# Performance work log

Measured on AMD Instinct MI355X. Metric: run time of the kernel, lower is better.

The kernel has to match this reference:

```python
import jax, jax.numpy as jnp
import numpy as np

B, N, D = 16, 512, 256   # batch, tokens(=input_size), emb_dim
H, DH = 8, 16            # heads, dim_head
INNER = H * DH           # 128
SCALE = DH ** -0.5
EPS = 1e-5


def _p(key, shape):
    return jax.random.normal(key, shape, dtype=jnp.float32) * 0.02


def setup_inputs() -> dict:
    key = jax.random.key(0)
    ks = jax.random.split(key, 12)
    inp = {
        "x": jax.random.normal(ks[0], (B, N, D), dtype=jnp.float32),
        # stage-1 attention (tokens=N, feat=D)
        "wqkv1": _p(ks[1], (D, 3 * INNER)),
        "wo1": _p(ks[2], (INNER, D)),
        "bo1": jnp.zeros((D,), jnp.float32),
        "ff1_w1": _p(ks[3], (D, 8 * D)),
        "ff1_b1": jnp.zeros((8 * D,), jnp.float32),
        "ff1_w2": _p(ks[4], (4 * D, D)),
        "ff1_b2": jnp.zeros((D,), jnp.float32),
        # stage-2 attention (tokens=D after transpose, feat=N=input_size)
        "wqkv2": _p(ks[5], (N, 3 * INNER)),
        "wo2": _p(ks[6], (INNER, N)),
        "bo2": jnp.zeros((N,), jnp.float32),
        "ff2_w1": _p(ks[7], (N, 8 * N)),
        "ff2_b1": jnp.zeros((8 * N,), jnp.float32),
        "ff2_w2": _p(ks[8], (4 * N, N)),
        "ff2_b2": jnp.zeros((N,), jnp.float32),
        # layernorms
        "ln1_g": jnp.ones((D,), jnp.float32), "ln1_b": jnp.zeros((D,), jnp.float32),
        "ln2_g": jnp.ones((D,), jnp.float32), "ln2_b": jnp.zeros((D,), jnp.float32),
        "ln3_g": jnp.ones((N,), jnp.float32), "ln3_b": jnp.zeros((N,), jnp.float32),
        "ln4_g": jnp.ones((N,), jnp.float32), "ln4_b": jnp.zeros((N,), jnp.float32),
    }
    return inp


def _layernorm(x, g, b):
    mu = jnp.mean(x, axis=-1, keepdims=True)
    var = jnp.mean(jnp.square(x - mu), axis=-1, keepdims=True)
    return (x - mu) * jax.lax.rsqrt(var + EPS) * g + b


def _attention(x, wqkv, wo, bo, share):
    b, n, _ = x.shape
    qkv = x @ wqkv                                 # [b, n, 3*INNER]
    q, k, v = jnp.split(qkv, 3, axis=-1)
    split_heads = lambda t: t.reshape(b, n, H, DH).transpose(0, 2, 1, 3)
    q, k, v = split_heads(q), split_heads(k), split_heads(v)
    energy = jnp.einsum('bhid,bhjd->bhij', q, k) * SCALE
    if share is not None:
        energy = energy + share
    attn = jax.nn.softmax(energy, axis=-1)
    out = jnp.einsum('bhij,bhjd->bhid', attn, v)   # [b, h, n, dh]
    out = out.transpose(0, 2, 1, 3).reshape(b, n, INNER)
    return out @ wo + bo, energy


def _geglu_ff(x, w1, b1, w2, b2):
    h = x @ w1 + b1
    a, g = jnp.split(h, 2, axis=-1)
    return (a * jax.nn.gelu(g, approximate=False)) @ w2 + b2


def reference(x, wqkv1, wo1, bo1, ff1_w1, ff1_b1, ff1_w2, ff1_b2,
              wqkv2, wo2, bo2, ff2_w1, ff2_b1, ff2_w2, ff2_b2,
              ln1_g, ln1_b, ln2_g, ln2_b, ln3_g, ln3_b, ln4_g, ln4_b):
    # stage 1: token attention + FFN
    attn_out, share = _attention(x, wqkv1, wo1, bo1, None)
    x = _layernorm(attn_out + x, ln1_g, ln1_b)
    x = _layernorm(_geglu_ff(x, ff1_w1, ff1_b1, ff1_w2, ff1_b2) + x, ln2_g, ln2_b)
    # stage 2: feature (column) attention + FFN on transposed x
    x = x.transpose(0, 2, 1)                       # [b, D, N]
    attn_out, share2 = _attention(x, wqkv2, wo2, bo2, None)
    x = _layernorm(attn_out + x, ln3_g, ln3_b)
    x = _layernorm(_geglu_ff(x, ff2_w1, ff2_b1, ff2_w2, ff2_b2) + x, ln4_g, ln4_b)
    x = x.transpose(0, 2, 1)                       # [b, N, D]
    return (x, share, share2)
```

## Files before the change

### kernel.cpp

```cpp
#include <hip/hip_runtime.h>
#include <cstddef>


typedef __attribute__((ext_vector_type(8))) short short8;
typedef __attribute__((ext_vector_type(4))) short bf16x4;
typedef __attribute__((ext_vector_type(4))) float f32x4;
typedef unsigned short u16t;

__device__ __forceinline__ u16t f2b(float f) {
  union { float f; unsigned u; } x; x.f = f;
  unsigned r = (x.u + 0x7fffu + ((x.u >> 16) & 1u)) >> 16;
  return (u16t)r;
}
__device__ __forceinline__ float b2f(u16t v) {
  union { unsigned u; float f; } x; x.u = ((unsigned)v) << 16;
  return x.f;
}

__device__ __forceinline__ void gload16(const void* g, void* l) {
  __builtin_amdgcn_global_load_lds(
      (const __attribute__((address_space(1))) void*)g,
      (__attribute__((address_space(3))) void*)l, 16, 0, 0);
}

__device__ __forceinline__ int origcol(int n, int halfN) {
  const int nb = n >> 7, s = (n >> 4) & 7, r = n & 15;
  return ((s & 1) ? halfN : 0) + (nb << 6) + ((s >> 1) << 4) + r;
}

template<int BN, int EPI>
__global__ __launch_bounds__(256) void mgemm(
    const u16t* __restrict__ A, const u16t* __restrict__ BT,
    const float* __restrict__ bias, const float* __restrict__ res,
    void* __restrict__ C, int M, int N, int K) {
  constexpr int WGC = (BN == 128) ? 2 : 1;
  constexpr int WM = (WGC == 2) ? 64 : 32;
  constexpr int MR = WM / 16;
  constexpr int NR = 4;
  constexpr int BISS = BN / 64;
  __shared__ u16t Al[128 * 32];
  __shared__ u16t Bl[BN * 32];
  const int t = threadIdx.x, lane = t & 63, wid = t >> 6;
  const int wr = (WGC == 2) ? (wid >> 1) : wid;
  const int wc = (WGC == 2) ? (wid & 1) : 0;
  const int lr = lane & 15, lq = lane >> 4;
  const int bm = blockIdx.y << 7, bn = blockIdx.x * BN;

  const int ao0 = wid * 2048 + lane * 16;
  const int ar0 = ao0 >> 6,          ac0 = (ao0 & 63) >> 1;
  const int ar1 = (ao0 + 1024) >> 6, ac1 = ((ao0 + 1024) & 63) >> 1;
  const int bo0 = wid * (1024 * BISS) + lane * 16;
  const int br0 = bo0 >> 6,          bc0 = (bo0 & 63) >> 1;
  const int br1 = (bo0 + 1024) >> 6, bc1 = ((bo0 + 1024) & 63) >> 1;

  const u16t* Ab = A + (size_t)bm * K;
  const u16t* Bb = BT + (size_t)bn * K;

  f32x4 acc[MR][NR];
#pragma unroll
  for (int m = 0; m < MR; ++m)
#pragma unroll
    for (int n = 0; n < NR; ++n) acc[m][n] = (f32x4){0.f, 0.f, 0.f, 0.f};

  for (int k0 = 0; k0 < K; k0 += 32) {
    gload16(Ab + (size_t)ar0 * K + k0 + ac0, (char*)Al + wid * 2048);
    gload16(Ab + (size_t)ar1 * K + k0 + ac1, (char*)Al + wid * 2048 + 1024);
    gload16(Bb + (size_t)br0 * K + k0 + bc0, (char*)Bl + wid * 1024 * BISS);
    if (BISS == 2)
      gload16(Bb + (size_t)br1 * K + k0 + bc1, (char*)Bl + wid * 2048 + 1024);
    __syncthreads();
    short8 af[MR], bf[NR];
#pragma unroll
    for (int m = 0; m < MR; ++m)
      af[m] = *(const short8*)&Al[(wr * WM + m * 16 + lr) * 32 + lq * 8];
#pragma unroll
    for (int n = 0; n < NR; ++n)
      bf[n] = *(const short8*)&Bl[(wc * 64 + n * 16 + lr) * 32 + lq * 8];
#pragma unroll
    for (int m = 0; m < MR; ++m)
#pragma unroll
      for (int n = 0; n < NR; ++n)
        acc[m][n] = __builtin_amdgcn_mfma_f32_16x16x32_bf16(af[m], bf[n], acc[m][n], 0, 0, 0);
    __syncthreads();
  }

  if (EPI == 2) {
    const int Nh = N >> 1;
#pragma unroll
    for (int np = 0; np < NR / 2; ++np) {
      const int ca = bn + wc * 64 + np * 32 + lr;
      const float ba = bias[ca], bg = bias[ca + 16];
      const int uc = (bn >> 1) + wc * 32 + np * 16 + lr;
#pragma unroll
      for (int m = 0; m < MR; ++m) {
#pragma unroll
        for (int i = 0; i < 4; ++i) {
          const int row = bm + wr * WM + m * 16 + lq * 4 + i;
          const float a = acc[m][2 * np][i] + ba;
          const float g = acc[m][2 * np + 1][i] + bg;
          const float ge = 0.5f * g * (1.f + erff(g * 0.70710678118654752f));
          ((u16t*)C)[(size_t)row * Nh + uc] = f2b(a * ge);
        }
      }
    }
  } else {
#pragma unroll
    for (int n = 0; n < NR; ++n) {
      const int col = bn + wc * 64 + n * 16 + lr;
      const float bv = bias ? bias[col] : 0.f;
#pragma unroll
      for (int m = 0; m < MR; ++m) {
#pragma unroll
        for (int i = 0; i < 4; ++i) {
          const int row = bm + wr * WM + m * 16 + lq * 4 + i;
          float v = acc[m][n][i] + bv;
          if (EPI == 1) {
            v += res[(size_t)row * N + col];
            ((float*)C)[(size_t)row * N + col] = v;
          } else {
            ((u16t*)C)[(size_t)row * N + col] = f2b(v);
          }
        }
      }
    }
  }
}

template<int NTOK>
__global__ __launch_bounds__(256) void attn_mfma(
    const u16t* __restrict__ qkv, float* __restrict__ share,
    u16t* __restrict__ outb) {
  __shared__ u16t VT[16][NTOK + 40];
  __shared__ u16t PB[4][16][40];
  const int t = threadIdx.x, lane = t & 63, wv = t >> 6;
  const int lr = lane & 15, lq = lane >> 4;
  const int bpb = NTOK / 64;
  const int bh = blockIdx.x / bpb, rg = blockIdx.x % bpb;
  const int b = bh >> 3, h = bh & 7;
  const u16t* qkvb = qkv + (size_t)b * NTOK * 384;

  for (int tok = t; tok < NTOK; tok += 256) {
    const u16t* vp = qkvb + (size_t)tok * 384 + 256 + h * 16;
    short8 v0 = *(const short8*)vp;
    short8 v1 = *(const short8*)(vp + 8);
#pragma unroll
    for (int d = 0; d < 8; ++d) {
      VT[d][tok]     = (u16t)v0[d];
      VT[d + 8][tok] = (u16t)v1[d];
    }
  }
  __syncthreads();

  const int i0 = rg * 64 + wv * 16;
  short8 qf = {0, 0, 0, 0, 0, 0, 0, 0};
  if (lq < 2)
    qf = *(const short8*)(qkvb + (size_t)(i0 + lr) * 384 + h * 16 + lq * 8);

  f32x4 oacc = {0.f, 0.f, 0.f, 0.f};
  f32x4 sacc = {0.f, 0.f, 0.f, 0.f};
  const f32x4 zero = {0.f, 0.f, 0.f, 0.f};
  float* shb = share + (size_t)bh * NTOK * NTOK;

  for (int t0 = 0; t0 < NTOK; t0 += 32) {
#pragma unroll
    for (int s2 = 0; s2 < 2; ++s2) {
      short8 kf = {0, 0, 0, 0, 0, 0, 0, 0};
      if (lq < 2)
        kf = *(const short8*)(qkvb + (size_t)(t0 + s2 * 16 + lr) * 384 + 128 + h * 16 + lq * 8);
      f32x4 e = __builtin_amdgcn_mfma_f32_16x16x32_bf16(qf, kf, zero, 0, 0, 0);
#pragma unroll
      for (int i = 0; i < 4; ++i) {
        const float ev = e[i] * 0.25f;
        shb[(size_t)(i0 + lq * 4 + i) * NTOK + t0 + s2 * 16 + lr] = ev;
        const float p = __expf(ev);
        sacc[i] += p;
        PB[wv][lq * 4 + i][s2 * 16 + lr] = f2b(p);
      }
    }
    asm volatile("s_waitcnt lgkmcnt(0)" ::: "memory");
    __builtin_amdgcn_sched_barrier(0);
    short8 pa = *(const short8*)&PB[wv][lr][lq * 8];
    short8 vf = *(const short8*)&VT[lr][t0 + lq * 8];
    oacc = __builtin_amdgcn_mfma_f32_16x16x32_bf16(pa, vf, oacc, 0, 0, 0);
    __builtin_amdgcn_sched_barrier(0);
  }
#pragma unroll
  for (int i = 0; i < 4; ++i) {
    float s = sacc[i];
    s += __shfl_xor(s, 1); s += __shfl_xor(s, 2);
    s += __shfl_xor(s, 4); s += __shfl_xor(s, 8);
    sacc[i] = s;
  }
#pragma unroll
  for (int i = 0; i < 4; ++i) {
    const float o = oacc[i] / sacc[i];
    outb[((size_t)(b * NTOK) + i0 + lq * 4 + i) * 128 + h * 16 + lr] = f2b(o);
  }
}

template<int NT, bool B16>
__global__ __launch_bounds__(NT) void ln_vec(
    const float* __restrict__ xin, const float* __restrict__ g,
    const float* __restrict__ be, float* __restrict__ y32,
    u16t* __restrict__ y16, int D) {
  const int row = blockIdx.x, t = threadIdx.x;
  const int lane = t & 63;
  const float4 x = ((const float4*)xin)[(size_t)row * (D >> 2) + t];
  float s = x.x + x.y + x.z + x.w;
  float s2 = x.x * x.x + x.y * x.y + x.z * x.z + x.w * x.w;
#pragma unroll
  for (int off = 32; off; off >>= 1) {
    s  += __shfl_xor(s, off);
    s2 += __shfl_xor(s2, off);
  }
  if (NT == 128) {
    __shared__ float a1[2], a2[2];
    const int wv = t >> 6;
    if (lane == 0) { a1[wv] = s; a2[wv] = s2; }
    __syncthreads();
    s = a1[0] + a1[1]; s2 = a2[0] + a2[1];
  }
  const float mean = s / D;
  const float var  = s2 / D - mean * mean;
  const float rstd = rsqrtf(var + 1e-5f);
  const float4 gv = ((const float4*)g)[t];
  const float4 bv = ((const float4*)be)[t];
  float4 y;
  y.x = (x.x - mean) * rstd * gv.x + bv.x;
  y.y = (x.y - mean) * rstd * gv.y + bv.y;
  y.z = (x.z - mean) * rstd * gv.z + bv.z;
  y.w = (x.w - mean) * rstd * gv.w + bv.w;
  ((float4*)y32)[(size_t)row * (D >> 2) + t] = y;
  if (B16) {
    bf16x4 p;
    p[0] = (short)f2b(y.x); p[1] = (short)f2b(y.y);
    p[2] = (short)f2b(y.z); p[3] = (short)f2b(y.w);
    *(bf16x4*)&y16[(size_t)row * D + t * 4] = p;
  }
}

template<bool BF16OUT>
__global__ void transp(const float* __restrict__ in, float* __restrict__ out32,
                       u16t* __restrict__ out16, int R, int C) {
  __shared__ float tile[32][33];
  const int b = blockIdx.z;
  const int r0 = blockIdx.y << 5, c0 = blockIdx.x << 5;
  const float* inb = in + (size_t)b * R * C;
  const int tx = threadIdx.x, ty = threadIdx.y;
#pragma unroll
  for (int dy = 0; dy < 32; dy += 8)
    tile[ty + dy][tx] = inb[(size_t)(r0 + ty + dy) * C + c0 + tx];
  __syncthreads();
#pragma unroll
  for (int dy = 0; dy < 32; dy += 8) {
    const float v = tile[tx][ty + dy];
    const size_t idx = (size_t)b * R * C + (size_t)(c0 + ty + dy) * R + r0 + tx;
    out32[idx] = v;
    if (BF16OUT) out16[idx] = f2b(v);
  }
}

__global__ __launch_bounds__(256) void prep_all(
    const float* __restrict__ x0, u16t* __restrict__ x16,
    const float* __restrict__ wqkv1, u16t* __restrict__ tqkv1,
    const float* __restrict__ wo1,   u16t* __restrict__ two1,
    const float* __restrict__ ff1w1, u16t* __restrict__ tff1a,
    const float* __restrict__ ff1w2, u16t* __restrict__ tff1b,
    const float* __restrict__ wqkv2, u16t* __restrict__ tqkv2,
    const float* __restrict__ wo2,   u16t* __restrict__ two2,
    const float* __restrict__ ff2w1, u16t* __restrict__ tff2a,
    const float* __restrict__ ff2w2, u16t* __restrict__ tff2b,
    const float* __restrict__ ff1b1, float* __restrict__ bp1,
    const float* __restrict__ ff2b1, float* __restrict__ bp2) {
  __shared__ float tile[32][33];
  const int b = blockIdx.x, t = threadIdx.x;
  const int tx = t & 31, ty = t >> 5;
  const float* src; u16t* dst;
  int K, N, bxd, blk, halfN = 0; bool perm = false;
  if (b < 1024) {
    const float* p = x0 + (size_t)(b * 256 + t) * 8;
    short8 v;
#pragma unroll
    for (int j = 0; j < 8; ++j) v[j] = (short)f2b(p[j]);
    *(short8*)(x16 + (size_t)(b * 256 + t) * 8) = v;
    return;
  } else if (b < 1120) { src = wqkv1; dst = tqkv1; K = 256;  N = 384;  bxd = 12;  blk = b - 1024; }
  else if (b < 1152)   { src = wo1;   dst = two1;  K = 128;  N = 256;  bxd = 8;   blk = b - 1120; }
  else if (b < 1664)   { src = ff1w1; dst = tff1a; K = 256;  N = 2048; bxd = 64;  blk = b - 1152; perm = true; halfN = 1024; }
  else if (b < 1920)   { src = ff1w2; dst = tff1b; K = 1024; N = 256;  bxd = 8;   blk = b - 1664; }
  else if (b < 2112)   { src = wqkv2; dst = tqkv2; K = 512;  N = 384;  bxd = 12;  blk = b - 1920; }
  else if (b < 2176)   { src = wo2;   dst = two2;  K = 128;  N = 512;  bxd = 16;  blk = b - 2112; }
  else if (b < 4224)   { src = ff2w1; dst = tff2a; K = 512;  N = 4096; bxd = 128; blk = b - 2176; perm = true; halfN = 2048; }
  else if (b < 5248)   { src = ff2w2; dst = tff2b; K = 2048; N = 512;  bxd = 16;  blk = b - 4224; }
  else if (b < 5256) { const int n = (b - 5248) * 256 + t; bp1[n] = ff1b1[origcol(n, 1024)]; return; }
  else               { const int n = (b - 5256) * 256 + t; bp2[n] = ff2b1[origcol(n, 2048)]; return; }

  const int bx = blk % bxd, by = blk / bxd;
  const int n0 = bx * 32, k0 = by * 32;
  const int nn = n0 + tx;
  const int no = perm ? origcol(nn, halfN) : nn;
#pragma unroll
  for (int dy = 0; dy < 32; dy += 8)
    tile[ty + dy][tx] = src[(size_t)(k0 + ty + dy) * N + no];
  __syncthreads();
#pragma unroll
  for (int dy = 0; dy < 32; dy += 8)
    dst[(size_t)(n0 + ty + dy) * K + k0 + tx] = f2b(tile[tx][ty + dy]);
}

extern "C" void kernel_launch(void* const* d_in, const int* in_sizes, int n_in,
                              void* d_out, int out_size, void* d_ws, size_t ws_size,
                              hipStream_t stream) {
  (void)in_sizes; (void)n_in; (void)out_size; (void)ws_size;
  const float* x0    = (const float*)d_in[0];
  const float* wqkv1 = (const float*)d_in[1];
  const float* wo1   = (const float*)d_in[2];
  const float* bo1   = (const float*)d_in[3];
  const float* ff1w1 = (const float*)d_in[4];
  const float* ff1b1 = (const float*)d_in[5];
  const float* ff1w2 = (const float*)d_in[6];
  const float* ff1b2 = (const float*)d_in[7];
  const float* wqkv2 = (const float*)d_in[8];
  const float* wo2   = (const float*)d_in[9];
  const float* bo2   = (const float*)d_in[10];
  const float* ff2w1 = (const float*)d_in[11];
  const float* ff2b1 = (const float*)d_in[12];
  const float* ff2w2 = (const float*)d_in[13];
  const float* ff2b2 = (const float*)d_in[14];
  const float* ln1g  = (const float*)d_in[15];
  const float* ln1b  = (const float*)d_in[16];
  const float* ln2g  = (const float*)d_in[17];
  const float* ln2b  = (const float*)d_in[18];
  const float* ln3g  = (const float*)d_in[19];
  const float* ln3b  = (const float*)d_in[20];
  const float* ln4g  = (const float*)d_in[21];
  const float* ln4b  = (const float*)d_in[22];

  float* out_x  = (float*)d_out;
  float* share1 = out_x + (size_t)2097152;
  float* share2 = share1 + (size_t)33554432;

  size_t off = 0;
  auto carve = [&](size_t bytes) -> void* {
    void* p = (char*)d_ws + off;
    off += (bytes + 255) & ~(size_t)255;
    return p;
  };
  u16t*  x16    = (u16t*)carve((size_t)8192 * 256 * 2);
  u16t*  qkv16  = (u16t*)carve((size_t)8192 * 384 * 2);
  u16t*  attn16 = (u16t*)carve((size_t)8192 * 128 * 2);
  float* sumb   = (float*)carve((size_t)8192 * 256 * 4);
  float* xa32   = (float*)carve((size_t)8192 * 256 * 4);
  u16t*  xa16   = (u16t*)carve((size_t)8192 * 256 * 2);
  float* xb32   = (float*)carve((size_t)8192 * 256 * 4);
  float* xt32   = (float*)carve((size_t)8192 * 256 * 4);
  u16t*  xt16   = (u16t*)carve((size_t)8192 * 256 * 2);
  float* xc32   = (float*)carve((size_t)8192 * 256 * 4);
  u16t*  xc16   = (u16t*)carve((size_t)8192 * 256 * 2);
  float* xd32   = (float*)carve((size_t)8192 * 256 * 4);
  u16t*  ubuf   = (u16t*)carve((size_t)4096 * 2048 * 2);
  u16t*  tqkv1  = (u16t*)carve((size_t)384 * 256 * 2);
  u16t*  two1   = (u16t*)carve((size_t)256 * 128 * 2);
  u16t*  tff1a  = (u16t*)carve((size_t)2048 * 256 * 2);
  u16t*  tff1b  = (u16t*)carve((size_t)256 * 1024 * 2);
  u16t*  tqkv2  = (u16t*)carve((size_t)384 * 512 * 2);
  u16t*  two2   = (u16t*)carve((size_t)512 * 128 * 2);
  u16t*  tff2a  = (u16t*)carve((size_t)4096 * 512 * 2);
  u16t*  tff2b  = (u16t*)carve((size_t)512 * 2048 * 2);
  float* bp1    = (float*)carve((size_t)2048 * 4);
  float* bp2    = (float*)carve((size_t)4096 * 4);

  const dim3 tb(32, 8);

  prep_all<<<5272, 256, 0, stream>>>(x0, x16, wqkv1, tqkv1, wo1, two1,
      ff1w1, tff1a, ff1w2, tff1b, wqkv2, tqkv2, wo2, two2,
      ff2w1, tff2a, ff2w2, tff2b, ff1b1, bp1, ff2b1, bp2);

  mgemm<64, 0><<<dim3(6, 64), 256, 0, stream>>>(x16, tqkv1, nullptr, nullptr, qkv16, 8192, 384, 256);
  attn_mfma<512><<<1024, 256, 0, stream>>>(qkv16, share1, attn16);
  mgemm<64, 1><<<dim3(4, 64), 256, 0, stream>>>(attn16, two1, bo1, x0, sumb, 8192, 256, 128);
  ln_vec<64, true><<<8192, 64, 0, stream>>>(sumb, ln1g, ln1b, xa32, xa16, 256);
  mgemm<128, 2><<<dim3(16, 64), 256, 0, stream>>>(xa16, tff1a, bp1, nullptr, ubuf, 8192, 2048, 256);
  mgemm<64, 1><<<dim3(4, 64), 256, 0, stream>>>(ubuf, tff1b, ff1b2, xa32, sumb, 8192, 256, 1024);
  ln_vec<64, false><<<8192, 64, 0, stream>>>(sumb, ln2g, ln2b, xb32, nullptr, 256);

  transp<true><<<dim3(8, 16, 16), tb, 0, stream>>>(xb32, xt32, xt16, 512, 256);

  mgemm<64, 0><<<dim3(6, 32), 256, 0, stream>>>(xt16, tqkv2, nullptr, nullptr, qkv16, 4096, 384, 512);
  attn_mfma<256><<<512, 256, 0, stream>>>(qkv16, share2, attn16);
  mgemm<64, 1><<<dim3(8, 32), 256, 0, stream>>>(attn16, two2, bo2, xt32, sumb, 4096, 512, 128);
  ln_vec<128, true><<<4096, 128, 0, stream>>>(sumb, ln3g, ln3b, xc32, xc16, 512);
  mgemm<128, 2><<<dim3(32, 32), 256, 0, stream>>>(xc16, tff2a, bp2, nullptr, ubuf, 4096, 4096, 512);
  mgemm<64, 1><<<dim3(8, 32), 256, 0, stream>>>(ubuf, tff2b, ff2b2, xc32, sumb, 4096, 512, 2048);
  ln_vec<128, false><<<4096, 128, 0, stream>>>(sumb, ln4g, ln4b, xd32, nullptr, 512);

  transp<false><<<dim3(16, 8, 16), tb, 0, stream>>>(xd32, out_x, nullptr, 256, 512);
}
```

Measured before the change: 230.4 us.

## Fuse residual layernorm into out-projection GEMMs and fold LN with transposes

Adds a gemmln kernel that runs the attention out-projection with bias, residual and full-row layernorm in one pass, replacing a GEMM plus a separate LN kernel in both stages. Adds an lnT kernel that applies layernorm and writes the transposed output in one kernel, replacing the LN+transpose pairs. Replaces erff in the GEGLU epilogue with an Abramowitz-Stegun polynomial using __expf. These cut kernel launches and fp32 round trips through memory. The cost is few blocks (128/256) in the fused GEMMs and a small approximation error in GELU.

```diff
diff --git a/kernel.cpp b/kernel.cpp
--- a/kernel.cpp
+++ b/kernel.cpp
@@ -3,7 +3,6 @@
 
 
 typedef __attribute__((ext_vector_type(8))) short short8;
-typedef __attribute__((ext_vector_type(4))) short bf16x4;
 typedef __attribute__((ext_vector_type(4))) float f32x4;
 typedef unsigned short u16t;
 
@@ -12,15 +11,21 @@
   unsigned r = (x.u + 0x7fffu + ((x.u >> 16) & 1u)) >> 16;
   return (u16t)r;
 }
-__device__ __forceinline__ float b2f(u16t v) {
-  union { unsigned u; float f; } x; x.u = ((unsigned)v) << 16;
-  return x.f;
-}
 
 __device__ __forceinline__ void gload16(const void* g, void* l) {
   __builtin_amdgcn_global_load_lds(
       (const __attribute__((address_space(1))) void*)g,
       (__attribute__((address_space(3))) void*)l, 16, 0, 0);
+}
+
+__device__ __forceinline__ float gelu_f(float g) {
+  const float x = g * 0.70710678118654752f;
+  const float ax = fabsf(x);
+  const float t = 1.f / (1.f + 0.3275911f * ax);
+  const float p = t * (0.254829592f + t * (-0.284496736f +
+                  t * (1.421413741f + t * (-1.453152027f + t * 1.061405429f))));
+  const float er = 1.f - p * __expf(-x * x);
+  return 0.5f * g * (1.f + copysignf(er, x));
 }
 
 __device__ __forceinline__ int origcol(int n, int halfN) {
@@ -98,8 +103,7 @@
           const int row = bm + wr * WM + m * 16 + lq * 4 + i;
           const float a = acc[m][2 * np][i] + ba;
           const float g = acc[m][2 * np + 1][i] + bg;
-          const float ge = 0.5f * g * (1.f + erff(g * 0.70710678118654752f));
-          ((u16t*)C)[(size_t)row * Nh + uc] = f2b(a * ge);
+          ((u16t*)C)[(size_t)row * Nh + uc] = f2b(a * gelu_f(g));
         }
       }
     }
@@ -123,6 +127,154 @@
         }
       }
     }
+  }
+}
+
+template<int NW>
+__global__ __launch_bounds__(256) void gemmln(
+    const u16t* __restrict__ A, const u16t* __restrict__ BT,
+    const float* __restrict__ bias, const float* __restrict__ res,
+    const float* __restrict__ g, const float* __restrict__ be,
+    float* __restrict__ y32, u16t* __restrict__ y16, int K) {
+  constexpr int NR = NW / 64;
+  __shared__ u16t Al[32 * 32];
+  __shared__ u16t Bl[NW * 32];
+  __shared__ float psum[4][32], psq[4][32];
+  const int t = threadIdx.x, lane = t & 63, wid = t >> 6;
+  const int lr = lane & 15, lq = lane >> 4;
+  const int bm = blockIdx.x << 5;
+  const int wofs = wid * (NW / 4);
+
+  f32x4 acc[2][NR];
+#pragma unroll
+  for (int m = 0; m < 2; ++m)
+#pragma unroll
+    for (int n = 0; n < NR; ++n) acc[m][n] = (f32x4){0.f, 0.f, 0.f, 0.f};
+
+  for (int k0 = 0; k0 < K; k0 += 32) {
+    if (wid < 2) {
+      const int c = wid * 64 + lane;
+      gload16(A + (size_t)(bm + (c >> 2)) * K + k0 + ((c & 3) << 3),
+              (char*)Al + wid * 1024);
+    }
+#pragma unroll
+    for (int j = 0; j < NW / 64; ++j) {
+      const int c = j * 256 + wid * 64 + lane;
+      gload16(BT + (size_t)(c >> 2) * K + k0 + ((c & 3) << 3),
+              (char*)Bl + (j * 256 + wid * 64) * 16);
+    }
+    __syncthreads();
+    short8 af[2], bf[NR];
+#pragma unroll
+    for (int m = 0; m < 2; ++m)
+      af[m] = *(const short8*)&Al[(m * 16 + lr) * 32 + lq * 8];
+#pragma unroll
+    for (int n = 0; n < NR; ++n)
+      bf[n] = *(const short8*)&Bl[(wofs + n * 16 + lr) * 32 + lq * 8];
+#pragma unroll
+    for (int m = 0; m < 2; ++m)
+#pragma unroll
+      for (int n = 0; n < NR; ++n)
+        acc[m][n] = __builtin_amdgcn_mfma_f32_16x16x32_bf16(af[m], bf[n], acc[m][n], 0, 0, 0);
+    __syncthreads();
+  }
+
+  float ps[2][4], ps2[2][4];
+#pragma unroll
+  for (int m = 0; m < 2; ++m)
+#pragma unroll
+    for (int i = 0; i < 4; ++i) { ps[m][i] = 0.f; ps2[m][i] = 0.f; }
+#pragma unroll
+  for (int m = 0; m < 2; ++m)
+#pragma unroll
+    for (int n = 0; n < NR; ++n) {
+      const int col = wofs + n * 16 + lr;
+      const float bv = bias[col];
+#pragma unroll
+      for (int i = 0; i < 4; ++i) {
+        const int row = bm + m * 16 + lq * 4 + i;
+        const float v = acc[m][n][i] + bv + res[(size_t)row * NW + col];
+        acc[m][n][i] = v;
+        ps[m][i] += v; ps2[m][i] += v * v;
+      }
+    }
+#pragma unroll
+  for (int m = 0; m < 2; ++m)
+#pragma unroll
+    for (int i = 0; i < 4; ++i) {
+      float s = ps[m][i], s2 = ps2[m][i];
+      s  += __shfl_xor(s, 1);  s  += __shfl_xor(s, 2);
+      s  += __shfl_xor(s, 4);  s  += __shfl_xor(s, 8);
+      s2 += __shfl_xor(s2, 1); s2 += __shfl_xor(s2, 2);
+      s2 += __shfl_xor(s2, 4); s2 += __shfl_xor(s2, 8);
+      if (lr == 0) {
+        psum[wid][m * 16 + lq * 4 + i] = s;
+        psq[wid][m * 16 + lq * 4 + i]  = s2;
+      }
+    }
+  __syncthreads();
+#pragma unroll
+  for (int m = 0; m < 2; ++m)
+#pragma unroll
+    for (int i = 0; i < 4; ++i) {
+      const int r = m * 16 + lq * 4 + i;
+      const float tot = psum[0][r] + psum[1][r] + psum[2][r] + psum[3][r];
+      const float tq  = psq[0][r]  + psq[1][r]  + psq[2][r]  + psq[3][r];
+      const float mean = tot / NW;
+      const float rstd = rsqrtf(tq / NW - mean * mean + 1e-5f);
+      const int row = bm + r;
+#pragma unroll
+      for (int n = 0; n < NR; ++n) {
+        const int col = wofs + n * 16 + lr;
+        const float y = (acc[m][n][i] - mean) * rstd * g[col] + be[col];
+        y32[(size_t)row * NW + col] = y;
+        y16[(size_t)row * NW + col] = f2b(y);
+      }
+    }
+}
+
+template<int CD, int RC, bool B16>
+__global__ __launch_bounds__(256) void lnT(
+    const float* __restrict__ in, const float* __restrict__ g,
+    const float* __restrict__ be, float* __restrict__ out32,
+    u16t* __restrict__ out16) {
+  __shared__ float tile[32][CD + 1];
+  __shared__ float smean[32], srstd[32];
+  const int t = threadIdx.x, lane = t & 63, wv = t >> 6;
+  const int r0 = blockIdx.x << 5;
+  const int b = r0 / RC, rl0 = r0 % RC;
+#pragma unroll 4
+  for (int r = 0; r < 32; ++r)
+    for (int c = t; c < CD; c += 256)
+      tile[r][c] = in[(size_t)(r0 + r) * CD + c];
+  __syncthreads();
+  for (int rr = 0; rr < 8; ++rr) {
+    const int r = wv * 8 + rr;
+    float s = 0.f, s2 = 0.f;
+#pragma unroll
+    for (int k = 0; k < CD / 64; ++k) {
+      const float v = tile[r][lane + k * 64];
+      s += v; s2 += v * v;
+    }
+#pragma unroll
+    for (int off = 32; off; off >>= 1) {
+      s += __shfl_xor(s, off); s2 += __shfl_xor(s2, off);
+    }
+    if (lane == 0) {
+      const float mean = s / CD;
+      smean[r] = mean;
+      srstd[r] = rsqrtf(s2 / CD - mean * mean + 1e-5f);
+    }
+  }
+  __syncthreads();
+  const int tx = t & 31, tc = t >> 5;
+  const float mean = smean[tx], rstd = srstd[tx];
+  for (int cc = 0; cc < CD / 8; ++cc) {
+    const int c = tc + cc * 8;
+    const float y = (tile[tx][c] - mean) * rstd * g[c] + be[c];
+    const size_t idx = ((size_t)b * CD + c) * RC + rl0 + tx;
+    out32[idx] = y;
+    if (B16) out16[idx] = f2b(y);
   }
 }
 
@@ -195,68 +347,6 @@
   for (int i = 0; i < 4; ++i) {
     const float o = oacc[i] / sacc[i];
     outb[((size_t)(b * NTOK) + i0 + lq * 4 + i) * 128 + h * 16 + lr] = f2b(o);
-  }
-}
-
-template<int NT, bool B16>
-__global__ __launch_bounds__(NT) void ln_vec(
-    const float* __restrict__ xin, const float* __restrict__ g,
-    const float* __restrict__ be, float* __restrict__ y32,
-    u16t* __restrict__ y16, int D) {
-  const int row = blockIdx.x, t = threadIdx.x;
-  const int lane = t & 63;
-  const float4 x = ((const float4*)xin)[(size_t)row * (D >> 2) + t];
-  float s = x.x + x.y + x.z + x.w;
-  float s2 = x.x * x.x + x.y * x.y + x.z * x.z + x.w * x.w;
-#pragma unroll
-  for (int off = 32; off; off >>= 1) {
-    s  += __shfl_xor(s, off);
-    s2 += __shfl_xor(s2, off);
-  }
-  if (NT == 128) {
-    __shared__ float a1[2], a2[2];
-    const int wv = t >> 6;
-    if (lane == 0) { a1[wv] = s; a2[wv] = s2; }
-    __syncthreads();
-    s = a1[0] + a1[1]; s2 = a2[0] + a2[1];
-  }
-  const float mean = s / D;
-  const float var  = s2 / D - mean * mean;
-  const float rstd = rsqrtf(var + 1e-5f);
-  const float4 gv = ((const float4*)g)[t];
-  const float4 bv = ((const float4*)be)[t];
-  float4 y;
-  y.x = (x.x - mean) * rstd * gv.x + bv.x;
-  y.y = (x.y - mean) * rstd * gv.y + bv.y;
-  y.z = (x.z - mean) * rstd * gv.z + bv.z;
-  y.w = (x.w - mean) * rstd * gv.w + bv.w;
-  ((float4*)y32)[(size_t)row * (D >> 2) + t] = y;
-  if (B16) {
-    bf16x4 p;
-    p[0] = (short)f2b(y.x); p[1] = (short)f2b(y.y);
-    p[2] = (short)f2b(y.z); p[3] = (short)f2b(y.w);
-    *(bf16x4*)&y16[(size_t)row * D + t * 4] = p;
-  }
-}
-
-template<bool BF16OUT>
-__global__ void transp(const float* __restrict__ in, float* __restrict__ out32,
-                       u16t* __restrict__ out16, int R, int C) {
-  __shared__ float tile[32][33];
-  const int b = blockIdx.z;
-  const int r0 = blockIdx.y << 5, c0 = blockIdx.x << 5;
-  const float* inb = in + (size_t)b * R * C;
-  const int tx = threadIdx.x, ty = threadIdx.y;
-#pragma unroll
-  for (int dy = 0; dy < 32; dy += 8)
-    tile[ty + dy][tx] = inb[(size_t)(r0 + ty + dy) * C + c0 + tx];
-  __syncthreads();
-#pragma unroll
-  for (int dy = 0; dy < 32; dy += 8) {
-    const float v = tile[tx][ty + dy];
-    const size_t idx = (size_t)b * R * C + (size_t)(c0 + ty + dy) * R + r0 + tx;
-    out32[idx] = v;
-    if (BF16OUT) out16[idx] = f2b(v);
   }
 }
 
@@ -352,13 +442,11 @@
   float* sumb   = (float*)carve((size_t)8192 * 256 * 4);
   float* xa32   = (float*)carve((size_t)8192 * 256 * 4);
   u16t*  xa16   = (u16t*)carve((size_t)8192 * 256 * 2);
-  float* xb32   = (float*)carve((size_t)8192 * 256 * 4);
   float* xt32   = (float*)carve((size_t)8192 * 256 * 4);
   u16t*  xt16   = (u16t*)carve((size_t)8192 * 256 * 2);
   float* xc32   = (float*)carve((size_t)8192 * 256 * 4);
   u16t*  xc16   = (u16t*)carve((size_t)8192 * 256 * 2);
-  float* xd32   = (float*)carve((size_t)8192 * 256 * 4);
-  u16t*  ubuf   = (u16t*)carve((size_t)4096 * 2048 * 2);
+  u16t*  ubuf   = (u16t*)carve((size_t)8192 * 1024 * 2);
   u16t*  tqkv1  = (u16t*)carve((size_t)384 * 256 * 2);
   u16t*  two1   = (u16t*)carve((size_t)256 * 128 * 2);
   u16t*  tff1a  = (u16t*)carve((size_t)2048 * 256 * 2);
@@ -370,29 +458,21 @@
   float* bp1    = (float*)carve((size_t)2048 * 4);
   float* bp2    = (float*)carve((size_t)4096 * 4);
 
-  const dim3 tb(32, 8);
-
   prep_all<<<5272, 256, 0, stream>>>(x0, x16, wqkv1, tqkv1, wo1, two1,
       ff1w1, tff1a, ff1w2, tff1b, wqkv2, tqkv2, wo2, two2,
       ff2w1, tff2a, ff2w2, tff2b, ff1b1, bp1, ff2b1, bp2);
 
   mgemm<64, 0><<<dim3(6, 64), 256, 0, stream>>>(x16, tqkv1, nullptr, nullptr, qkv16, 8192, 384, 256);
   attn_mfma<512><<<1024, 256, 0, stream>>>(qkv16, share1, attn16);
-  mgemm<64, 1><<<dim3(4, 64), 256, 0, stream>>>(attn16, two1, bo1, x0, sumb, 8192, 256, 128);
-  ln_vec<64, true><<<8192, 64, 0, stream>>>(sumb, ln1g, ln1b, xa32, xa16, 256);
+  gemmln<256><<<256, 256, 0, stream>>>(attn16, two1, bo1, x0, ln1g, ln1b, xa32, xa16, 128);
   mgemm<128, 2><<<dim3(16, 64), 256, 0, stream>>>(xa16, tff1a, bp1, nullptr, ubuf, 8192, 2048, 256);
   mgemm<64, 1><<<dim3(4, 64), 256, 0, stream>>>(ubuf, tff1b, ff1b2, xa32, sumb, 8192, 256, 1024);
-  ln_vec<64, false><<<8192, 64, 0, stream>>>(sumb, ln2g, ln2b, xb32, nullptr, 256);
-
-  transp<true><<<dim3(8, 16, 16), tb, 0, stream>>>(xb32, xt32, xt16, 512, 256);
+  lnT<256, 512, true><<<256, 256, 0, stream>>>(sumb, ln2g, ln2b, xt32, xt16);
 
   mgemm<64, 0><<<dim3(6, 32), 256, 0, stream>>>(xt16, tqkv2, nullptr, nullptr, qkv16, 4096, 384, 512);
   attn_mfma<256><<<512, 256, 0, stream>>>(qkv16, share2, attn16);
-  mgemm<64, 1><<<dim3(8, 32), 256, 0, stream>>>(attn16, two2, bo2, xt32, sumb, 4096, 512, 128);
-  ln_vec<128, true><<<4096, 128, 0, stream>>>(sumb, ln3g, ln3b, xc32, xc16, 512);
+  gemmln<512><<<128, 256, 0, stream>>>(attn16, two2, bo2, xt32, ln3g, ln3b, xc32, xc16, 128);
   mgemm<128, 2><<<dim3(32, 32), 256, 0, stream>>>(xc16, tff2a, bp2, nullptr, ubuf, 4096, 4096, 512);
   mgemm<64, 1><<<dim3(8, 32), 256, 0, stream>>>(ubuf, tff2b, ff2b2, xc32, sumb, 4096, 512, 2048);
-  ln_vec<128, false><<<4096, 128, 0, stream>>>(sumb, ln4g, ln4b, xd32, nullptr, 512);
-
-  transp<false><<<dim3(16, 8, 16), tb, 0, stream>>>(xd32, out_x, nullptr, 256, 512);
-}
+  lnT<512, 256, false><<<128, 256, 0, stream>>>(sumb, ln4g, ln4b, out_x, nullptr);
+}
```

New measurement: 248.0 us. 7.6% more time.

## Add 64x64-tile GEMM for narrow matmuls and use polynomial erf in GEGLU

Applied to the files above, without the earlier changes.

Adds a new mgemm64 kernel with 64x64 output tiles and a 2x2 wave layout. It is used for the QKV, output-projection and FFN down-projection GEMMs, so these narrow-N GEMMs launch twice as many blocks to fill the CUs. The up-projection GEMM keeps only the 128x128 variant. The GEGLU epilogue replaces erff with an Abramowitz-Stegun polynomial plus __expf, which cuts transcendental cost but adds about 1e-7 absolute error in erf. Smaller tiles reduce data reuse per block and increase global traffic.

```diff
diff --git a/kernel.cpp b/kernel.cpp
--- a/kernel.cpp
+++ b/kernel.cpp
@@ -12,10 +12,6 @@
   unsigned r = (x.u + 0x7fffu + ((x.u >> 16) & 1u)) >> 16;
   return (u16t)r;
 }
-__device__ __forceinline__ float b2f(u16t v) {
-  union { unsigned u; float f; } x; x.u = ((unsigned)v) << 16;
-  return x.f;
-}
 
 __device__ __forceinline__ void gload16(const void* g, void* l) {
   __builtin_amdgcn_global_load_lds(
@@ -23,63 +19,63 @@
       (__attribute__((address_space(3))) void*)l, 16, 0, 0);
 }
 
+__device__ __forceinline__ float gelu_f(float g) {
+  const float x = g * 0.70710678118654752f;
+  const float ax = fabsf(x);
+  const float t = 1.f / (1.f + 0.3275911f * ax);
+  const float p = t * (0.254829592f + t * (-0.284496736f +
+                  t * (1.421413741f + t * (-1.453152027f + t * 1.061405429f))));
+  const float er = 1.f - p * __expf(-x * x);
+  return 0.5f * g * (1.f + copysignf(er, x));
+}
+
 __device__ __forceinline__ int origcol(int n, int halfN) {
   const int nb = n >> 7, s = (n >> 4) & 7, r = n & 15;
   return ((s & 1) ? halfN : 0) + (nb << 6) + ((s >> 1) << 4) + r;
 }
 
-template<int BN, int EPI>
+template<int EPI>
 __global__ __launch_bounds__(256) void mgemm(
     const u16t* __restrict__ A, const u16t* __restrict__ BT,
     const float* __restrict__ bias, const float* __restrict__ res,
     void* __restrict__ C, int M, int N, int K) {
-  constexpr int WGC = (BN == 128) ? 2 : 1;
-  constexpr int WM = (WGC == 2) ? 64 : 32;
-  constexpr int MR = WM / 16;
-  constexpr int NR = 4;
-  constexpr int BISS = BN / 64;
   __shared__ u16t Al[128 * 32];
-  __shared__ u16t Bl[BN * 32];
+  __shared__ u16t Bl[128 * 32];
   const int t = threadIdx.x, lane = t & 63, wid = t >> 6;
-  const int wr = (WGC == 2) ? (wid >> 1) : wid;
-  const int wc = (WGC == 2) ? (wid & 1) : 0;
+  const int wr = wid >> 1, wc = wid & 1;
   const int lr = lane & 15, lq = lane >> 4;
-  const int bm = blockIdx.y << 7, bn = blockIdx.x * BN;
+  const int bm = blockIdx.y << 7, bn = blockIdx.x << 7;
 
   const int ao0 = wid * 2048 + lane * 16;
   const int ar0 = ao0 >> 6,          ac0 = (ao0 & 63) >> 1;
   const int ar1 = (ao0 + 1024) >> 6, ac1 = ((ao0 + 1024) & 63) >> 1;
-  const int bo0 = wid * (1024 * BISS) + lane * 16;
-  const int br0 = bo0 >> 6,          bc0 = (bo0 & 63) >> 1;
-  const int br1 = (bo0 + 1024) >> 6, bc1 = ((bo0 + 1024) & 63) >> 1;
 
   const u16t* Ab = A + (size_t)bm * K;
   const u16t* Bb = BT + (size_t)bn * K;
 
-  f32x4 acc[MR][NR];
-#pragma unroll
-  for (int m = 0; m < MR; ++m)
-#pragma unroll
-    for (int n = 0; n < NR; ++n) acc[m][n] = (f32x4){0.f, 0.f, 0.f, 0.f};
+  f32x4 acc[4][4];
+#pragma unroll
+  for (int m = 0; m < 4; ++m)
+#pragma unroll
+    for (int n = 0; n < 4; ++n) acc[m][n] = (f32x4){0.f, 0.f, 0.f, 0.f};
 
   for (int k0 = 0; k0 < K; k0 += 32) {
     gload16(Ab + (size_t)ar0 * K + k0 + ac0, (char*)Al + wid * 2048);
     gload16(Ab + (size_t)ar1 * K + k0 + ac1, (char*)Al + wid * 2048 + 1024);
-    gload16(Bb + (size_t)br0 * K + k0 + bc0, (char*)Bl + wid * 1024 * BISS);
-    if (BISS == 2)
-      gload16(Bb + (size_t)br1 * K + k0 + bc1, (char*)Bl + wid * 2048 + 1024);
+    gload16(Bb + (size_t)ar0 * K + k0 + ac0, (char*)Bl + wid * 2048);
+    gload16(Bb + (size_t)ar1 * K + k0 + ac1, (char*)Bl + wid * 2048 + 1024);
     __syncthreads();
-    short8 af[MR], bf[NR];
-#pragma unroll
-    for (int m = 0; m < MR; ++m)
-      af[m] = *(const short8*)&Al[(wr * WM + m * 16 + lr) * 32 + lq * 8];
-#pragma unroll
-    for (int n = 0; n < NR; ++n)
+    short8 af[4], bf[4];
+#pragma unroll
+    for (int m = 0; m < 4; ++m)
+      af[m] = *(const short8*)&Al[(wr * 64 + m * 16 + lr) * 32 + lq * 8];
+#pragma unroll
+    for (int n = 0; n < 4; ++n)
       bf[n] = *(const short8*)&Bl[(wc * 64 + n * 16 + lr) * 32 + lq * 8];
 #pragma unroll
-    for (int m = 0; m < MR; ++m)
-#pragma unroll
-      for (int n = 0; n < NR; ++n)
+    for (int m = 0; m < 4; ++m)
+#pragma unroll
+      for (int n = 0; n < 4; ++n)
         acc[m][n] = __builtin_amdgcn_mfma_f32_16x16x32_bf16(af[m], bf[n], acc[m][n], 0, 0, 0);
     __syncthreads();
   }
@@ -87,32 +83,31 @@
   if (EPI == 2) {
     const int Nh = N >> 1;
 #pragma unroll
-    for (int np = 0; np < NR / 2; ++np) {
+    for (int np = 0; np < 2; ++np) {
       const int ca = bn + wc * 64 + np * 32 + lr;
       const float ba = bias[ca], bg = bias[ca + 16];
       const int uc = (bn >> 1) + wc * 32 + np * 16 + lr;
 #pragma unroll
-      for (int m = 0; m < MR; ++m) {
+      for (int m = 0; m < 4; ++m) {
 #pragma unroll
         for (int i = 0; i < 4; ++i) {
-          const int row = bm + wr * WM + m * 16 + lq * 4 + i;
+          const int row = bm + wr * 64 + m * 16 + lq * 4 + i;
           const float a = acc[m][2 * np][i] + ba;
           const float g = acc[m][2 * np + 1][i] + bg;
-          const float ge = 0.5f * g * (1.f + erff(g * 0.70710678118654752f));
-          ((u16t*)C)[(size_t)row * Nh + uc] = f2b(a * ge);
+          ((u16t*)C)[(size_t)row * Nh + uc] = f2b(a * gelu_f(g));
         }
       }
     }
   } else {
 #pragma unroll
-    for (int n = 0; n < NR; ++n) {
+    for (int n = 0; n < 4; ++n) {
       const int col = bn + wc * 64 + n * 16 + lr;
       const float bv = bias ? bias[col] : 0.f;
 #pragma unroll
-      for (int m = 0; m < MR; ++m) {
+      for (int m = 0; m < 4; ++m) {
 #pragma unroll
         for (int i = 0; i < 4; ++i) {
-          const int row = bm + wr * WM + m * 16 + lq * 4 + i;
+          const int row = bm + wr * 64 + m * 16 + lq * 4 + i;
           float v = acc[m][n][i] + bv;
           if (EPI == 1) {
             v += res[(size_t)row * N + col];
@@ -120,6 +115,69 @@
           } else {
             ((u16t*)C)[(size_t)row * N + col] = f2b(v);
           }
+        }
+      }
+    }
+  }
+}
+
+template<int EPI>
+__global__ __launch_bounds__(256) void mgemm64(
+    const u16t* __restrict__ A, const u16t* __restrict__ BT,
+    const float* __restrict__ bias, const float* __restrict__ res,
+    void* __restrict__ C, int M, int N, int K) {
+  __shared__ u16t Al[64 * 32];
+  __shared__ u16t Bl[64 * 32];
+  const int t = threadIdx.x, lane = t & 63, wid = t >> 6;
+  const int wr = wid >> 1, wc = wid & 1;
+  const int lr = lane & 15, lq = lane >> 4;
+  const int bm = blockIdx.y << 6, bn = blockIdx.x << 6;
+  const int ch = wid * 64 + lane;
+  const int crow = ch >> 2, ccol = (ch & 3) << 3;
+
+  const u16t* Ab = A + (size_t)bm * K;
+  const u16t* Bb = BT + (size_t)bn * K;
+
+  f32x4 acc[2][2];
+#pragma unroll
+  for (int m = 0; m < 2; ++m)
+#pragma unroll
+    for (int n = 0; n < 2; ++n) acc[m][n] = (f32x4){0.f, 0.f, 0.f, 0.f};
+
+  for (int k0 = 0; k0 < K; k0 += 32) {
+    gload16(Ab + (size_t)crow * K + k0 + ccol, (char*)Al + wid * 1024);
+    gload16(Bb + (size_t)crow * K + k0 + ccol, (char*)Bl + wid * 1024);
+    __syncthreads();
+    short8 af[2], bf[2];
+#pragma unroll
+    for (int m = 0; m < 2; ++m)
+      af[m] = *(const short8*)&Al[(wr * 32 + m * 16 + lr) * 32 + lq * 8];
+#pragma unroll
+    for (int n = 0; n < 2; ++n)
+      bf[n] = *(const short8*)&Bl[(wc * 32 + n * 16 + lr) * 32 + lq * 8];
+#pragma unroll
+    for (int m = 0; m < 2; ++m)
+#pragma unroll
+      for (int n = 0; n < 2; ++n)
+        acc[m][n] = __builtin_amdgcn_mfma_f32_16x16x32_bf16(af[m], bf[n], acc[m][n], 0, 0, 0);
+    __syncthreads();
+  }
+
+#pragma unroll
+  for (int n = 0; n < 2; ++n) {
+    const int col = bn + wc * 32 + n * 16 + lr;
+    const float bv = bias ? bias[col] : 0.f;
+#pragma unroll
+    for (int m = 0; m < 2; ++m) {
+#pragma unroll
+      for (int i = 0; i < 4; ++i) {
+        const int row = bm + wr * 32 + m * 16 + lq * 4 + i;
+        float v = acc[m][n][i] + bv;
+        if (EPI == 1) {
+          v += res[(size_t)row * N + col];
+          ((float*)C)[(size_t)row * N + col] = v;
+        } else {
+          ((u16t*)C)[(size_t)row * N + col] = f2b(v);
         }
       }
     }
@@ -358,7 +416,7 @@
   float* xc32   = (float*)carve((size_t)8192 * 256 * 4);
   u16t*  xc16   = (u16t*)carve((size_t)8192 * 256 * 2);
   float* xd32   = (float*)carve((size_t)8192 * 256 * 4);
-  u16t*  ubuf   = (u16t*)carve((size_t)4096 * 2048 * 2);
+  u16t*  ubuf   = (u16t*)carve((size_t)8192 * 1024 * 2);
   u16t*  tqkv1  = (u16t*)carve((size_t)384 * 256 * 2);
   u16t*  two1   = (u16t*)carve((size_t)256 * 128 * 2);
   u16t*  tff1a  = (u16t*)carve((size_t)2048 * 256 * 2);
@@ -370,29 +428,27 @@
   float* bp1    = (float*)carve((size_t)2048 * 4);
   float* bp2    = (float*)carve((size_t)4096 * 4);
 
-  const dim3 tb(32, 8);
-
   prep_all<<<5272, 256, 0, stream>>>(x0, x16, wqkv1, tqkv1, wo1, two1,
       ff1w1, tff1a, ff1w2, tff1b, wqkv2, tqkv2, wo2, two2,
       ff2w1, tff2a, ff2w2, tff2b, ff1b1, bp1, ff2b1, bp2);
 
-  mgemm<64, 0><<<dim3(6, 64), 256, 0, stream>>>(x16, tqkv1, nullptr, nullptr, qkv16, 8192, 384, 256);
+  mgemm64<0><<<dim3(6, 128), 256, 0, stream>>>(x16, tqkv1, nullptr, nullptr, qkv16, 8192, 384, 256);
   attn_mfma<512><<<1024, 256, 0, stream>>>(qkv16, share1, attn16);
-  mgemm<64, 1><<<dim3(4, 64), 256, 0, stream>>>(attn16, two1, bo1, x0, sumb, 8192, 256, 128);
+  mgemm64<1><<<dim3(4, 128), 256, 0, stream>>>(attn16, two1, bo1, x0, sumb, 8192, 256, 128);
   ln_vec<64, true><<<8192, 64, 0, stream>>>(sumb, ln1g, ln1b, xa32, xa16, 256);
-  mgemm<128, 2><<<dim3(16, 64), 256, 0, stream>>>(xa16, tff1a, bp1, nullptr, ubuf, 8192, 2048, 256);
-  mgemm<64, 1><<<dim3(4, 64), 256, 0, stream>>>(ubuf, tff1b, ff1b2, xa32, sumb, 8192, 256, 1024);
+  mgemm<2><<<dim3(16, 64), 256, 0, stream>>>(xa16, tff1a, bp1, nullptr, ubuf, 8192, 2048, 256);
+  mgemm64<1><<<dim3(4, 128), 256, 0, stream>>>(ubuf, tff1b, ff1b2, xa32, sumb, 8192, 256, 1024);
   ln_vec<64, false><<<8192, 64, 0, stream>>>(sumb, ln2g, ln2b, xb32, nullptr, 256);
 
-  transp<true><<<dim3(8, 16, 16), tb, 0, stream>>>(xb32, xt32, xt16, 512, 256);
-
-  mgemm<64, 0><<<dim3(6, 32), 256, 0, stream>>>(xt16, tqkv2, nullptr, nullptr, qkv16, 4096, 384, 512);
+  transp<true><<<dim3(8, 16, 16), dim3(32, 8), 0, stream>>>(xb32, xt32, xt16, 512, 256);
+
+  mgemm64<0><<<dim3(6, 64), 256, 0, stream>>>(xt16, tqkv2, nullptr, nullptr, qkv16, 4096, 384, 512);
   attn_mfma<256><<<512, 256, 0, stream>>>(qkv16, share2, attn16);
-  mgemm<64, 1><<<dim3(8, 32), 256, 0, stream>>>(attn16, two2, bo2, xt32, sumb, 4096, 512, 128);
+  mgemm64<1><<<dim3(8, 64), 256, 0, stream>>>(attn16, two2, bo2, xt32, sumb, 4096, 512, 128);
   ln_vec<128, true><<<4096, 128, 0, stream>>>(sumb, ln3g, ln3b, xc32, xc16, 512);
-  mgemm<128, 2><<<dim3(32, 32), 256, 0, stream>>>(xc16, tff2a, bp2, nullptr, ubuf, 4096, 4096, 512);
-  mgemm<64, 1><<<dim3(8, 32), 256, 0, stream>>>(ubuf, tff2b, ff2b2, xc32, sumb, 4096, 512, 2048);
+  mgemm<2><<<dim3(32, 32), 256, 0, stream>>>(xc16, tff2a, bp2, nullptr, ubuf, 4096, 4096, 512);
+  mgemm64<1><<<dim3(8, 64), 256, 0, stream>>>(ubuf, tff2b, ff2b2, xc32, sumb, 4096, 512, 2048);
   ln_vec<128, false><<<4096, 128, 0, stream>>>(sumb, ln4g, ln4b, xd32, nullptr, 512);
 
-  transp<false><<<dim3(16, 8, 16), tb, 0, stream>>>(xd32, out_x, nullptr, 256, 512);
-}
+  transp<false><<<dim3(16, 8, 16), dim3(32, 8), 0, stream>>>(xd32, out_x, nullptr, 256, 512);
+}
```

After: 215.6 us. 6.4% less time.
